# Kernel optimization log

Measured on AMD Instinct MI355X. Metric: run time of the kernel, lower is better.

## Reference

```python
import jax, jax.numpy as jnp
import numpy as np

B, D, N = 1024, 2048, 16384
TEMP, LAMBDA2, MU = 0.05, 0.5, 1.0
EPS = 1e-12


def l2norm(x):
    # F.normalize(x, dim=1): x / max(||x||, eps)
    n = jnp.sqrt(jnp.sum(x * x, axis=1, keepdims=True))
    return x / jnp.maximum(n, EPS)


def cdist(x, f):
    # Euclidean distance matrix [B, N]
    x2 = jnp.sum(x * x, axis=1, keepdims=True)          # [B,1]
    f2 = jnp.sum(f * f, axis=1)                          # [N]
    sq = x2 + f2[None, :] - 2.0 * (x @ f.T)
    return jnp.sqrt(jnp.maximum(sq, 0.0))


def cross_entropy(logits, targets):
    logp = jax.nn.log_softmax(logits, axis=1)
    return -jnp.mean(logp[jnp.arange(logits.shape[0]), targets])


def setup_inputs() -> dict:
    key = jax.random.key(0)
    ks = jax.random.split(key, 10)
    inp = {
        'inputs': jax.random.normal(ks[0], (B, D), jnp.float32),
        'inputs_up': jax.random.normal(ks[1], (B, D), jnp.float32),
        'inputs_down': jax.random.normal(ks[2], (B, D), jnp.float32),
        'inputs_teacher': jax.random.normal(ks[3], (B, D), jnp.float32),
        'inputs_up_teacher': jax.random.normal(ks[4], (B, D), jnp.float32),
        'inputs_down_teacher': jax.random.normal(ks[5], (B, D), jnp.float32),
        'targets': jax.random.randint(ks[6], (B,), 0, N, jnp.int32),
        'epoch': 1,
        # memory bank buffers (unit-normalized rows, as maintained by CM updates)
        'features': l2norm(jax.random.normal(ks[7], (N, D), jnp.float32)),
        'features_up': l2norm(jax.random.normal(ks[8], (N, D), jnp.float32)),
        'features_down': l2norm(jax.random.normal(ks[9], (N, D), jnp.float32)),
    }
    return inp


def reference(inputs, inputs_up, inputs_down, inputs_teacher, inputs_up_teacher,
              inputs_down_teacher, targets, epoch, features, features_up, features_down):
    x = l2norm(inputs)
    xu = l2norm(inputs_up)
    xd = l2norm(inputs_down)
    t = l2norm(inputs_teacher)
    tu = l2norm(inputs_up_teacher)
    td = l2norm(inputs_down_teacher)

    # softmax over Euclidean distances to memory (used as 'logits' for CE below)
    x_soft = jax.nn.softmax(cdist(x, features), axis=1)
    xu_soft = jax.nn.softmax(cdist(xu, features_up), axis=1)
    xd_soft = jax.nn.softmax(cdist(xd, features_down), axis=1)

    # CM forward: similarity logits against memory, scaled by temperature
    out = (x @ features.T) / TEMP
    out_u = (xu @ features_up.T) / TEMP
    out_d = (xd @ features_down.T) / TEMP

    # MSELoss(reduce=False)(a,b).mean(0).sum()
    ld = jnp.sum(jnp.mean((x - t) ** 2, axis=0))
    ld_u = jnp.sum(jnp.mean((xu - tu) ** 2, axis=0))
    ld_d = jnp.sum(jnp.mean((xd - td) ** 2, axis=0))

    loss = ((1.0 - LAMBDA2) * (cross_entropy(out, targets) + MU * ld + cross_entropy(x_soft, targets))
            + LAMBDA2 * (cross_entropy(out_u, targets) + MU * ld_u + cross_entropy(xu_soft, targets))
            + LAMBDA2 * (cross_entropy(out_d, targets) + MU * ld_d + cross_entropy(xd_soft, targets)))
    return loss
```

## Files before the change

kernel.cpp:

```cpp
#include <hip/hip_runtime.h>

constexpr int BB = 1024;
constexpr int DD = 2048;
constexpr int NN = 16384;
constexpr float TEMP   = 0.05f;
constexpr float LAMBDA2 = 0.5f;
constexpr float MU      = 1.0f;
constexpr float EPSN    = 1e-12f;

typedef __bf16  bf16x8  __attribute__((ext_vector_type(8)));
typedef unsigned short ushort8 __attribute__((ext_vector_type(8)));
typedef float   floatx4 __attribute__((ext_vector_type(4)));

__device__ inline unsigned short f32_to_bf16(float f) {
  unsigned int u = __builtin_bit_cast(unsigned int, f);
  u += 0x7fffu + ((u >> 16) & 1u);
  return (unsigned short)(u >> 16);
}

__device__ inline float block_sum256(float v, float* sbuf) {
#pragma unroll
  for (int o = 32; o > 0; o >>= 1) v += __shfl_down(v, o, 64);
  int lane = threadIdx.x & 63, w = threadIdx.x >> 6;
  __syncthreads();
  if (lane == 0) sbuf[w] = v;
  __syncthreads();
  return sbuf[0] + sbuf[1] + sbuf[2] + sbuf[3];
}

__device__ inline float block_max256(float v, float* sbuf) {
#pragma unroll
  for (int o = 32; o > 0; o >>= 1) v = fmaxf(v, __shfl_down(v, o, 64));
  int lane = threadIdx.x & 63, w = threadIdx.x >> 6;
  __syncthreads();
  if (lane == 0) sbuf[w] = v;
  __syncthreads();
  return fmaxf(fmaxf(sbuf[0], sbuf[1]), fmaxf(sbuf[2], sbuf[3]));
}

__global__ void __launch_bounds__(256) norm_mse_kernel(
    const float* __restrict__ X, const float* __restrict__ T,
    unsigned short* __restrict__ Xb, float* __restrict__ mse_part) {
  __shared__ float sbuf[4];
  const int b = blockIdx.x;
  const float4* xr = (const float4*)(X + (size_t)b * DD);
  const float4* tr = (const float4*)(T + (size_t)b * DD);
  float4 xv[2], tv[2];
  float sx = 0.f, st = 0.f;
#pragma unroll
  for (int i = 0; i < 2; ++i) {
    int idx = i * 256 + threadIdx.x;
    xv[i] = xr[idx];  tv[i] = tr[idx];
    sx += xv[i].x*xv[i].x + xv[i].y*xv[i].y + xv[i].z*xv[i].z + xv[i].w*xv[i].w;
    st += tv[i].x*tv[i].x + tv[i].y*tv[i].y + tv[i].z*tv[i].z + tv[i].w*tv[i].w;
  }
  sx = block_sum256(sx, sbuf);
  st = block_sum256(st, sbuf);
  const float rx = 1.f / fmaxf(sqrtf(sx), EPSN);
  const float rt = 1.f / fmaxf(sqrtf(st), EPSN);
  float ms = 0.f;
  ushort4* xb4 = (ushort4*)(Xb + (size_t)b * DD);
#pragma unroll
  for (int i = 0; i < 2; ++i) {
    int idx = i * 256 + threadIdx.x;
    float xn, tn, d;
    ushort4 o;
    xn = xv[i].x * rx; tn = tv[i].x * rt; d = xn - tn; ms += d * d; o.x = f32_to_bf16(xn);
    xn = xv[i].y * rx; tn = tv[i].y * rt; d = xn - tn; ms += d * d; o.y = f32_to_bf16(xn);
    xn = xv[i].z * rx; tn = tv[i].z * rt; d = xn - tn; ms += d * d; o.z = f32_to_bf16(xn);
    xn = xv[i].w * rx; tn = tv[i].w * rt; d = xn - tn; ms += d * d; o.w = f32_to_bf16(xn);
    xb4[idx] = o;
  }
  ms = block_sum256(ms, sbuf);
  if (threadIdx.x == 0) mse_part[b] = ms;
}

__global__ void __launch_bounds__(256) feat_convert_kernel(
    const float* __restrict__ F, unsigned short* __restrict__ Fb) {
  const int stride = gridDim.x * 256;
  const float4* fr = (const float4*)F;
  constexpr int TOT = NN * DD / 8;
  for (int i = blockIdx.x * 256 + threadIdx.x; i < TOT; i += stride) {
    float4 a = fr[i * 2], b = fr[i * 2 + 1];
    ushort8 o;
    o[0] = f32_to_bf16(a.x); o[1] = f32_to_bf16(a.y);
    o[2] = f32_to_bf16(a.z); o[3] = f32_to_bf16(a.w);
    o[4] = f32_to_bf16(b.x); o[5] = f32_to_bf16(b.y);
    o[6] = f32_to_bf16(b.z); o[7] = f32_to_bf16(b.w);
    *(ushort8*)(Fb + (size_t)i * 8) = o;
  }
}

constexpr int BM = 128, BN = 128, BK = 64;

__device__ inline void async_copy16(const void* g, void* l) {
  __builtin_amdgcn_global_load_lds(
      (const __attribute__((address_space(1))) unsigned int*)g,
      (__attribute__((address_space(3))) unsigned int*)l, 16, 0, 0);
}

__global__ void __launch_bounds__(256) gemm_bt_kernel(
    const unsigned short* __restrict__ A,
    const unsigned short* __restrict__ Bm,
    float* __restrict__ C) {
  __shared__ __align__(16) unsigned short As[BM * BK];
  __shared__ __align__(16) unsigned short Bs[BN * BK];

  const int tid  = threadIdx.x;
  const int lane = tid & 63;
  const int wave = tid >> 6;
  const int quad = lane >> 4;
  const int l16  = lane & 15;
  const int wm = (wave >> 1) * 64;
  const int wn = (wave & 1) * 64;
  const int m0 = blockIdx.y * BM;
  const int n0 = blockIdx.x * BN;

  const unsigned short* gsrc[8];
  unsigned short* ldst[8];
#pragma unroll
  for (int c = 0; c < 8; ++c) {
    const int e  = c * 256 + tid;
    const int ei = (c < 4) ? e : e - 1024;
    const int row = ei >> 3;
    const int sc  = ei & 7;
    const int tc  = sc ^ (row & 7);
    const unsigned short* base =
        (c < 4) ? (A + (size_t)(m0 + row) * DD) : (Bm + (size_t)(n0 + row) * DD);
    gsrc[c] = base + tc * 8;
    ldst[c] = ((c < 4) ? As : Bs) + ei * 8;
  }

  const unsigned short* aRd[2][4];
  const unsigned short* bRd[2][4];
#pragma unroll
  for (int s = 0; s < 2; ++s) {
    const int sc = (s * 4 + quad) ^ (l16 & 7);
#pragma unroll
    for (int r = 0; r < 4; ++r) {
      aRd[s][r] = &As[(wm + r * 16 + l16) * BK + sc * 8];
      bRd[s][r] = &Bs[(wn + r * 16 + l16) * BK + sc * 8];
    }
  }

  floatx4 acc[4][4] = {};

  for (int k0 = 0; k0 < DD; k0 += BK) {
#pragma unroll
    for (int c = 0; c < 8; ++c) {
      async_copy16(gsrc[c], ldst[c]);
      gsrc[c] += BK;
    }
    __syncthreads();

#pragma unroll
    for (int s = 0; s < 2; ++s) {
      bf16x8 af[4], bf[4];
#pragma unroll
      for (int r = 0; r < 4; ++r) {
        af[r] = __builtin_bit_cast(bf16x8, *(const ushort8*)aRd[s][r]);
        bf[r] = __builtin_bit_cast(bf16x8, *(const ushort8*)bRd[s][r]);
      }
#pragma unroll
      for (int r = 0; r < 4; ++r)
#pragma unroll
        for (int c = 0; c < 4; ++c)
          acc[r][c] = __builtin_amdgcn_mfma_f32_16x16x32_bf16(af[r], bf[c], acc[r][c], 0, 0, 0);
    }
    __syncthreads();
  }

#pragma unroll
  for (int r = 0; r < 4; ++r) {
    const int grow = m0 + wm + r * 16 + quad * 4;
#pragma unroll
    for (int c = 0; c < 4; ++c) {
      const int gcol = n0 + wn + c * 16 + l16;
#pragma unroll
      for (int i = 0; i < 4; ++i)
        C[(size_t)(grow + i) * NN + gcol] = acc[r][c][i];
    }
  }
}

__global__ void __launch_bounds__(256) rowstat_kernel(
    const float* __restrict__ sim, const int* __restrict__ tgt,
    float* __restrict__ ce_part) {
  __shared__ float sbuf[4];
  const int b = blockIdx.x;
  const float4* sr = (const float4*)(sim + (size_t)b * NN);
  constexpr float INV_T = 1.0f / TEMP;

  float4 dv[16];
  float m1 = -1e30f, s1 = 0.f;
  float m2 = -1e30f;
#pragma unroll
  for (int i = 0; i < 16; ++i) {
    const int idx = i * 256 + threadIdx.x;
    float4 s = sr[idx];
    float lm = fmaxf(fmaxf(s.x, s.y), fmaxf(s.z, s.w)) * INV_T;
    if (lm > m1) { s1 *= expf(m1 - lm); m1 = lm; }
    s1 += expf(s.x * INV_T - m1) + expf(s.y * INV_T - m1)
        + expf(s.z * INV_T - m1) + expf(s.w * INV_T - m1);
    float4 d;
    d.x = sqrtf(fmaxf(2.f - 2.f * s.x, 0.f));
    d.y = sqrtf(fmaxf(2.f - 2.f * s.y, 0.f));
    d.z = sqrtf(fmaxf(2.f - 2.f * s.z, 0.f));
    d.w = sqrtf(fmaxf(2.f - 2.f * s.w, 0.f));
    dv[i] = d;
    m2 = fmaxf(m2, fmaxf(fmaxf(d.x, d.y), fmaxf(d.z, d.w)));
  }
  const float M1 = block_max256(m1, sbuf);
  const float s1t = block_sum256(s1 * expf(m1 - M1), sbuf);
  const float M2 = block_max256(m2, sbuf);

  float s2 = 0.f;
#pragma unroll
  for (int i = 0; i < 16; ++i) {
    float4 d = dv[i];
    s2 += expf(d.x - M2) + expf(d.y - M2) + expf(d.z - M2) + expf(d.w - M2);
  }
  const float s2t = block_sum256(s2, sbuf);
  const float invs2 = 1.f / s2t;

  float sp = 0.f;
#pragma unroll
  for (int i = 0; i < 16; ++i) {
    float4 d = dv[i];
    sp += expf(expf(d.x - M2) * invs2) + expf(expf(d.y - M2) * invs2)
        + expf(expf(d.z - M2) * invs2) + expf(expf(d.w - M2) * invs2);
  }
  const float spt = block_sum256(sp, sbuf);

  if (threadIdx.x == 0) {
    const int t = tgt[b];
    const float st = sim[(size_t)b * NN + t];
    const float dt = sqrtf(fmaxf(2.f - 2.f * st, 0.f));
    const float pt = expf(dt - M2) * invs2;
    const float ce1 = M1 + logf(s1t) - st * INV_T;
    const float ce2 = logf(spt) - pt;
    ce_part[b] = ce1 + ce2;
  }
}

__global__ void __launch_bounds__(256) final_reduce_kernel(
    const float* __restrict__ mse_part,
    const float* __restrict__ ce_part,
    float* __restrict__ loss) {
  __shared__ float sbuf[4];
  float s = 0.f;
  for (int i = threadIdx.x; i < 3 * BB; i += 256) {
    const float w = (i < BB) ? (1.0f - LAMBDA2) : LAMBDA2;
    s += w * (MU * mse_part[i] + ce_part[i]);
  }
  s = block_sum256(s, sbuf);
  if (threadIdx.x == 0) loss[0] = s * (1.0f / (float)BB);
}

extern "C" void kernel_launch(void* const* d_in, const int* in_sizes, int n_in,
                              void* d_out, int out_size, void* d_ws, size_t ws_size,
                              hipStream_t stream) {
  const float* xin[3] = {(const float*)d_in[0], (const float*)d_in[1], (const float*)d_in[2]};
  const float* tin[3] = {(const float*)d_in[3], (const float*)d_in[4], (const float*)d_in[5]};
  const int*   targets = (const int*)d_in[6];
  const float* fin[3] = {(const float*)d_in[8], (const float*)d_in[9], (const float*)d_in[10]};

  char* ws = (char*)d_ws;
  size_t off = 0;
  unsigned short* featb = (unsigned short*)(ws + off); off += (size_t)NN * DD * 2;
  float*          sim   = (float*)(ws + off);          off += (size_t)BB * NN * 4;
  unsigned short* xb    = (unsigned short*)(ws + off); off += (size_t)BB * DD * 2;
  float*          msep  = (float*)(ws + off);          off += (size_t)3 * BB * 4;
  float*          cep   = (float*)(ws + off);          off += (size_t)3 * BB * 4;

  for (int i = 0; i < 3; ++i) {
    norm_mse_kernel<<<BB, 256, 0, stream>>>(xin[i], tin[i], xb, msep + i * BB);
    feat_convert_kernel<<<4096, 256, 0, stream>>>(fin[i], featb);
    gemm_bt_kernel<<<dim3(NN / BN, BB / BM), 256, 0, stream>>>(xb, featb, sim);
    rowstat_kernel<<<BB, 256, 0, stream>>>(sim, targets, cep + i * BB);
  }
  final_reduce_kernel<<<1, 256, 0, stream>>>(msep, cep, (float*)d_out);
}
```

Before: 731.6 us.

## Rewrite bf16 GEMM with 256x256 tiles, 8 waves and double-buffered LDS prefetch

Measured after the change: 752.9 us. +2.9%, slower.

```diff
diff --git a/kernel.cpp b/kernel.cpp
--- a/kernel.cpp
+++ b/kernel.cpp
@@ -91,7 +91,8 @@
   }
 }
 
-constexpr int BM = 128, BN = 128, BK = 64;
+constexpr int BM = 256, BN = 256, BK = 64;
+constexpr int KT = DD / BK;
 
 __device__ inline void async_copy16(const void* g, void* l) {
   __builtin_amdgcn_global_load_lds(
@@ -99,86 +100,110 @@
       (__attribute__((address_space(3))) unsigned int*)l, 16, 0, 0);
 }
 
-__global__ void __launch_bounds__(256) gemm_bt_kernel(
+__device__ __forceinline__ void stage_half(const unsigned short* src,
+                                           unsigned short* dstRegion, int tid8) {
+  async_copy16(src, dstRegion + tid8);
+  async_copy16(src + 64 * DD, dstRegion + 4096 + tid8);
+}
+
+__global__ void __launch_bounds__(512, 2) gemm_bt_kernel(
     const unsigned short* __restrict__ A,
     const unsigned short* __restrict__ Bm,
     float* __restrict__ C) {
-  __shared__ __align__(16) unsigned short As[BM * BK];
-  __shared__ __align__(16) unsigned short Bs[BN * BK];
+  __shared__ __align__(16) unsigned short As[2 * 2 * 128 * 64];
+  __shared__ __align__(16) unsigned short Bs[2 * 2 * 128 * 64];
 
   const int tid  = threadIdx.x;
   const int lane = tid & 63;
   const int wave = tid >> 6;
+  const int l16  = lane & 15;
   const int quad = lane >> 4;
-  const int l16  = lane & 15;
-  const int wm = (wave >> 1) * 64;
-  const int wn = (wave & 1) * 64;
+  const int rm   = wave >> 2;
+  const int rn   = wave & 3;
   const int m0 = blockIdx.y * BM;
   const int n0 = blockIdx.x * BN;
 
-  const unsigned short* gsrc[8];
-  unsigned short* ldst[8];
-#pragma unroll
-  for (int c = 0; c < 8; ++c) {
-    const int e  = c * 256 + tid;
-    const int ei = (c < 4) ? e : e - 1024;
-    const int row = ei >> 3;
-    const int sc  = ei & 7;
-    const int tc  = sc ^ (row & 7);
-    const unsigned short* base =
-        (c < 4) ? (A + (size_t)(m0 + row) * DD) : (Bm + (size_t)(n0 + row) * DD);
-    gsrc[c] = base + tc * 8;
-    ldst[c] = ((c < 4) ? As : Bs) + ei * 8;
-  }
-
-  const unsigned short* aRd[2][4];
-  const unsigned short* bRd[2][4];
-#pragma unroll
-  for (int s = 0; s < 2; ++s) {
-    const int sc = (s * 4 + quad) ^ (l16 & 7);
-#pragma unroll
-    for (int r = 0; r < 4; ++r) {
-      aRd[s][r] = &As[(wm + r * 16 + l16) * BK + sc * 8];
-      bRd[s][r] = &Bs[(wn + r * 16 + l16) * BK + sc * 8];
+  const int xr = l16 & 7;
+  const int cs[2] = { (quad ^ xr) * 8, ((4 + quad) ^ xr) * 8 };
+
+  const int srow = tid >> 3;
+  const int lcol = ((tid & 7) ^ (srow & 7)) * 8;
+  const int tid8 = tid * 8;
+  const unsigned short* aSrcT = A  + (size_t)(m0 + srow) * DD + lcol;
+  const unsigned short* bSrcT = Bm + (size_t)(n0 + srow) * DD + lcol;
+
+  floatx4 acc[8][4] = {};
+
+  stage_half(aSrcT,                As,          tid8);
+  stage_half(aSrcT + 128 * DD,     As + 8192,   tid8);
+  stage_half(bSrcT,                Bs,          tid8);
+  stage_half(bSrcT + 128 * DD,     Bs + 8192,   tid8);
+  stage_half(bSrcT + BK,           Bs + 16384,  tid8);
+  stage_half(bSrcT + 128 * DD + BK, Bs + 24576, tid8);
+  asm volatile("s_waitcnt vmcnt(4)" ::: "memory");
+  asm volatile("s_barrier" ::: "memory");
+
+  for (int t = 0; t < KT; ++t) {
+    const int c = t & 1, o = c ^ 1;
+    const unsigned short* aB = As + c * 16384 + rm * 8192 + l16 * 64;
+    const unsigned short* bB = Bs + c * 16384 + (rn >> 1) * 8192
+                                  + (rn & 1) * 4096 + l16 * 64;
+    const int kA = (t + 1 < KT) ? (t + 1) * BK : 0;
+    const int kB = (t + 2 < KT) ? (t + 2) * BK : 0;
+    const unsigned short* aS = aSrcT + kA;
+    const unsigned short* bS = bSrcT + kB;
+
+    const unsigned short* stSrc[4] = { aS, aS + 128 * DD, bS, bS + 128 * DD };
+    unsigned short* stDst[4] = { As + o * 16384, As + o * 16384 + 8192,
+                                 Bs + c * 16384, Bs + c * 16384 + 8192 };
+
+    bf16x8 bf[4][2];
+#pragma unroll
+    for (int mp = 0; mp < 4; ++mp) {
+      if (mp == 0) {
+#pragma unroll
+        for (int n = 0; n < 4; ++n)
+#pragma unroll
+          for (int s = 0; s < 2; ++s)
+            bf[n][s] = __builtin_bit_cast(bf16x8,
+                         *(const ushort8*)(bB + n * 1024 + cs[s]));
+      }
+      bf16x8 af[2][2];
+#pragma unroll
+      for (int mi = 0; mi < 2; ++mi)
+#pragma unroll
+        for (int s = 0; s < 2; ++s)
+          af[mi][s] = __builtin_bit_cast(bf16x8,
+                        *(const ushort8*)(aB + (mp * 2 + mi) * 1024 + cs[s]));
+
+      stage_half(stSrc[mp], stDst[mp], tid8);
+
+      asm volatile("s_barrier" ::: "memory");
+      __builtin_amdgcn_s_setprio(1);
+#pragma unroll
+      for (int mi = 0; mi < 2; ++mi)
+#pragma unroll
+        for (int n = 0; n < 4; ++n)
+#pragma unroll
+          for (int s = 0; s < 2; ++s)
+            acc[mp * 2 + mi][n] = __builtin_amdgcn_mfma_f32_16x16x32_bf16(
+                af[mi][s], bf[n][s], acc[mp * 2 + mi][n], 0, 0, 0);
+      __builtin_amdgcn_s_setprio(0);
+      if (mp == 3)
+        asm volatile("s_waitcnt vmcnt(4)" ::: "memory");
+      asm volatile("s_barrier" ::: "memory");
     }
   }
 
-  floatx4 acc[4][4] = {};
-
-  for (int k0 = 0; k0 < DD; k0 += BK) {
-#pragma unroll
-    for (int c = 0; c < 8; ++c) {
-      async_copy16(gsrc[c], ldst[c]);
-      gsrc[c] += BK;
-    }
-    __syncthreads();
-
-#pragma unroll
-    for (int s = 0; s < 2; ++s) {
-      bf16x8 af[4], bf[4];
-#pragma unroll
-      for (int r = 0; r < 4; ++r) {
-        af[r] = __builtin_bit_cast(bf16x8, *(const ushort8*)aRd[s][r]);
-        bf[r] = __builtin_bit_cast(bf16x8, *(const ushort8*)bRd[s][r]);
-      }
-#pragma unroll
-      for (int r = 0; r < 4; ++r)
-#pragma unroll
-        for (int c = 0; c < 4; ++c)
-          acc[r][c] = __builtin_amdgcn_mfma_f32_16x16x32_bf16(af[r], bf[c], acc[r][c], 0, 0, 0);
-    }
-    __syncthreads();
-  }
-
-#pragma unroll
-  for (int r = 0; r < 4; ++r) {
-    const int grow = m0 + wm + r * 16 + quad * 4;
-#pragma unroll
-    for (int c = 0; c < 4; ++c) {
-      const int gcol = n0 + wn + c * 16 + l16;
+#pragma unroll
+  for (int r = 0; r < 8; ++r) {
+    const int grow = m0 + rm * 128 + r * 16 + quad * 4;
+#pragma unroll
+    for (int n = 0; n < 4; ++n) {
+      const int gcol = n0 + rn * 64 + n * 16 + l16;
 #pragma unroll
       for (int i = 0; i < 4; ++i)
-        C[(size_t)(grow + i) * NN + gcol] = acc[r][c][i];
+        C[(size_t)(grow + i) * NN + gcol] = acc[r][n][i];
     }
   }
 }
@@ -276,7 +301,7 @@
   for (int i = 0; i < 3; ++i) {
     norm_mse_kernel<<<BB, 256, 0, stream>>>(xin[i], tin[i], xb, msep + i * BB);
     feat_convert_kernel<<<4096, 256, 0, stream>>>(fin[i], featb);
-    gemm_bt_kernel<<<dim3(NN / BN, BB / BM), 256, 0, stream>>>(xb, featb, sim);
+    gemm_bt_kernel<<<dim3(NN / BN, BB / BM), 512, 0, stream>>>(xb, featb, sim);
     rowstat_kernel<<<BB, 256, 0, stream>>>(sim, targets, cep + i * BB);
   }
   final_reduce_kernel<<<1, 256, 0, stream>>>(msep, cep, (float*)d_out);
```
